# Optimization experiments

Hardware: AMD Instinct MI355X
Metric: run time of the kernel (lower is better)

The kernel has to match this reference:

```python
import jax, jax.numpy as jnp
import numpy as np

N_NODES = 50000
N_EDGES = 800000
IN_C = 512
OUT_C = 256
DEC_D = 256
MASK_RATE = 0.5
NUM_MASK = int(N_NODES * MASK_RATE)


def _gcn_conv(h_in, W, b, src, dst, dinv, n):
    # PyG GCNConv: add self-loops, symmetric normalization D^-1/2 (A+I) D^-1/2
    h = h_in @ W                                   # [N, out]
    coef = (dinv[src] * dinv[dst])[:, None]        # [E, 1]
    agg = jax.ops.segment_sum(h[src] * coef, dst, num_segments=n)
    agg = agg + h * (dinv * dinv)[:, None]         # self-loop term
    return agg + b


def setup_inputs() -> dict:
    key = jax.random.key(0)
    ks = jax.random.split(key, 9)
    x = jax.random.normal(ks[0], (N_NODES, IN_C), dtype=jnp.float32)
    edge_index = jax.random.randint(ks[1], (2, N_EDGES), 0, N_NODES, dtype=jnp.int32)
    perm = jax.random.permutation(ks[2], N_NODES)
    mask_indices = perm[:NUM_MASK].astype(jnp.int32)
    mask_token = jax.random.normal(ks[3], (1, IN_C), dtype=jnp.float32)
    s_enc = 1.0 / np.sqrt(IN_C)
    enc_W = jax.random.uniform(ks[4], (IN_C, OUT_C), jnp.float32, -s_enc, s_enc)
    enc_b = jnp.zeros((OUT_C,), jnp.float32)
    s_dec = 1.0 / np.sqrt(OUT_C)
    dec_W = jax.random.uniform(ks[5], (OUT_C, DEC_D), jnp.float32, -s_dec, s_dec)
    dec_b = jnp.zeros((DEC_D,), jnp.float32)
    s_mlp = 1.0 / np.sqrt(DEC_D)
    mlp_W = jax.random.uniform(ks[6], (DEC_D, IN_C), jnp.float32, -s_mlp, s_mlp)
    mlp_b = jax.random.uniform(ks[7], (IN_C,), jnp.float32, -s_mlp, s_mlp)
    return {"x": x, "edge_index": edge_index, "mask_indices": mask_indices,
            "mask_token": mask_token, "enc_W": enc_W, "enc_b": enc_b,
            "dec_W": dec_W, "dec_b": dec_b, "mlp_W": mlp_W, "mlp_b": mlp_b}


def reference(x, edge_index, mask_indices, mask_token, enc_W, enc_b, dec_W, dec_b, mlp_W, mlp_b):
    src, dst = edge_index[0], edge_index[1]
    n = x.shape[0]
    # degree with self-loops (shared by both GCN layers)
    deg = jax.ops.segment_sum(jnp.ones((N_EDGES,), x.dtype), dst, num_segments=n) + 1.0
    dinv = jax.lax.rsqrt(deg)
    # mask nodes: replace masked rows with learned mask token
    x_masked = x.at[mask_indices].set(mask_token[0])
    # encoder: GCNConv(in_c -> out_c)
    z = _gcn_conv(x_masked, enc_W, enc_b, src, dst, dinv, n)
    # decoder: GCNConv(out_c -> dec_d) -> relu -> linear(dec_d -> in_c)
    h = jax.nn.relu(_gcn_conv(z, dec_W, dec_b, src, dst, dinv, n))
    x_recon = h @ mlp_W + mlp_b
    return (x_recon, x, mask_indices)
```

## Files before the change

kernel.cpp:

```cpp
#include <hip/hip_runtime.h>
#include <math.h>

#define NNODES 50000
#define NEDGES 800000
#define INC 512
#define OUTC 256
#define DECD 256
#define NMASK 25000

#define SCAN_B 1024
#define NSCAN ((NNODES + SCAN_B - 1) / SCAN_B)

#define PB_CVT   25000
#define PB_DEG   (PB_CVT + 3125)
#define PB_MASK  (PB_DEG + 98)
#define PB_WT    (PB_MASK + 1280)
#define PB_TOK   (PB_WT + 64)

typedef __attribute__((ext_vector_type(8))) short short8;
typedef __attribute__((ext_vector_type(4))) float f32x4;

__device__ __forceinline__ unsigned short f2bf(float f) {
    unsigned int u = __float_as_uint(f);
    u = (u + 0x7fff + ((u >> 16) & 1)) >> 16;
    return (unsigned short)u;
}
__device__ __forceinline__ float bf2f(unsigned short u) {
    return __uint_as_float(((unsigned int)u) << 16);
}


__global__ __launch_bounds__(256) void prep_k(const float4* __restrict__ x4,
                                              float4* __restrict__ outx,
                                              ushort4* __restrict__ xbf,
                                              const int* __restrict__ dst, int* __restrict__ deg,
                                              const int* __restrict__ midx,
                                              float* __restrict__ out_mask,
                                              unsigned* __restrict__ maskbits,
                                              const float* __restrict__ encW,
                                              const float* __restrict__ decW,
                                              const float* __restrict__ mlpW,
                                              unsigned short* __restrict__ encWt,
                                              unsigned short* __restrict__ decWt,
                                              unsigned short* __restrict__ mlpWt,
                                              const float* __restrict__ token,
                                              float* __restrict__ tokh) {
    int b = blockIdx.x, tid = threadIdx.x;
    if (b < PB_CVT) {
        int i = b * 256 + tid;
        float4 v = x4[i];
        outx[i] = v;
        ushort4 u;
        u.x = f2bf(v.x); u.y = f2bf(v.y); u.z = f2bf(v.z); u.w = f2bf(v.w);
        xbf[i] = u;
    } else if (b < PB_DEG) {
        int e = (b - PB_CVT) * 256 + tid;
        atomicAdd(&deg[dst[e]], 1);
    } else if (b < PB_MASK) {
        int i = (b - PB_DEG) * 256 + tid;
        if (i < NMASK) {
            int r = midx[i];
            out_mask[i] = (float)r;
            atomicOr(&maskbits[r >> 5], 1u << (r & 31));
        }
    } else if (b < PB_WT) {
        int o = (b - PB_MASK) * 256 + tid;
        if (o < 131072) {
            int n = o >> 9, k = o & 511;
            encWt[o] = f2bf(encW[(size_t)k * OUTC + n]);
        } else if (o < 196608) {
            int o2 = o - 131072;
            int n = o2 >> 8, k = o2 & 255;
            decWt[o2] = f2bf(decW[(size_t)k * DECD + n]);
        } else {
            int o2 = o - 196608;
            int n = o2 >> 8, k = o2 & 255;
            mlpWt[o2] = f2bf(mlpW[(size_t)k * INC + n]);
        }
    } else {
        int b2 = b - PB_WT;
        int j = b2 * 4 + (tid >> 6);
        int l = tid & 63;
        float s = 0.f;
#pragma unroll
        for (int i = 0; i < INC / 64; ++i) {
            int k = i * 64 + l;
            s += token[k] * encW[(size_t)k * OUTC + j];
        }
#pragma unroll
        for (int d = 32; d > 0; d >>= 1) s += __shfl_down(s, d, 64);
        if (l == 0) tokh[j] = s;
    }
}


__global__ __launch_bounds__(1024) void scan_part_k(const int* __restrict__ deg,
                                                    int* __restrict__ bsum,
                                                    float* __restrict__ dinv) {
    int i = blockIdx.x * SCAN_B + threadIdx.x;
    int v = (i < NNODES) ? deg[i] : 0;
    if (i < NNODES) dinv[i] = rsqrtf((float)v + 1.0f);
    int lane = threadIdx.x & 63, w = threadIdx.x >> 6;
    int s = v;
#pragma unroll
    for (int d = 32; d > 0; d >>= 1) s += __shfl_down(s, d, 64);
    __shared__ int ws[16];
    if (lane == 0) ws[w] = s;
    __syncthreads();
    if (threadIdx.x == 0) {
        int tot = 0;
#pragma unroll
        for (int j = 0; j < 16; ++j) tot += ws[j];
        bsum[blockIdx.x] = tot;
    }
}

__global__ __launch_bounds__(64) void scan_carry_k(const int* __restrict__ bsum,
                                                   int* __restrict__ bcarry,
                                                   int* __restrict__ offs) {
    int t = threadIdx.x;
    int v = (t < NSCAN) ? bsum[t] : 0;
    int incl = v;
#pragma unroll
    for (int d = 1; d < 64; d <<= 1) {
        int u = __shfl_up(incl, d, 64);
        if (t >= d) incl += u;
    }
    if (t < NSCAN) bcarry[t] = incl - v;
    if (t == 63) offs[NNODES] = incl;
}

__global__ __launch_bounds__(1024) void scan_fin_k(const int* __restrict__ deg,
                                                   const int* __restrict__ bcarry,
                                                   int* __restrict__ offs,
                                                   int* __restrict__ cursor) {
    int i = blockIdx.x * SCAN_B + threadIdx.x;
    int v = (i < NNODES) ? deg[i] : 0;
    int lane = threadIdx.x & 63, w = threadIdx.x >> 6;
    int incl = v;
#pragma unroll
    for (int d = 1; d < 64; d <<= 1) {
        int u = __shfl_up(incl, d, 64);
        if (lane >= d) incl += u;
    }
    __shared__ int ws[16];
    if (lane == 63) ws[w] = incl;
    __syncthreads();
    int carry = bcarry[blockIdx.x];
    for (int j = 0; j < w; ++j) carry += ws[j];
    int ex = carry + incl - v;
    if (i < NNODES) { offs[i] = ex; cursor[i] = ex; }
}

__global__ void fill_csr_k(const int* __restrict__ src, const int* __restrict__ dst,
                           const float* __restrict__ dinv, int* __restrict__ cursor,
                           int2* __restrict__ edges) {
    int e = blockIdx.x * blockDim.x + threadIdx.x;
    if (e >= NEDGES) return;
    int s = src[e], d = dst[e];
    int pos = atomicAdd(&cursor[d], 1);
    edges[pos] = make_int2(s, __float_as_int(dinv[s] * dinv[d]));
}


__global__ __launch_bounds__(256) void gemm_bf16_k(const unsigned short* __restrict__ A,
                                                   const unsigned short* __restrict__ Bt,
                                                   void* __restrict__ Cout,
                                                   int M, int K, int N,
                                                   const float* __restrict__ bias,
                                                   int out_bf16,
                                                   const unsigned* __restrict__ maskbits,
                                                   const float* __restrict__ tokh) {
    __shared__ unsigned short As[128 * 32];
    __shared__ unsigned short Bs[128 * 32];
    const int t = threadIdx.x;
    const int lane = t & 63, wv = t >> 6;
    const int bm = blockIdx.y * 128;
    const int bn = blockIdx.x * 128;
    const int wm = (wv >> 1) * 64, wn = (wv & 1) * 64;
    const int lr = lane & 15, lq = lane >> 4;

    f32x4 acc[4][4] = {};

    for (int k0 = 0; k0 < K; k0 += 32) {
        __syncthreads();
#pragma unroll
        for (int r = 0; r < 2; ++r) {
            int idx = r * 256 + wv * 64 + lane;
            int row = idx >> 2;
            int c8 = (idx & 3) * 8;
            int ga = bm + row;
            if (ga >= M) ga = M - 1;
            const unsigned short* gA = A + (size_t)ga * K + k0 + c8;
            const unsigned short* gB = Bt + (size_t)(bn + row) * K + k0 + c8;
            __builtin_amdgcn_global_load_lds(
                (const __attribute__((address_space(1))) unsigned int*)gA,
                (__attribute__((address_space(3))) unsigned int*)&As[(r * 256 + wv * 64) * 8],
                16, 0, 0);
            __builtin_amdgcn_global_load_lds(
                (const __attribute__((address_space(1))) unsigned int*)gB,
                (__attribute__((address_space(3))) unsigned int*)&Bs[(r * 256 + wv * 64) * 8],
                16, 0, 0);
        }
        __syncthreads();

        short8 av[4], bv[4];
#pragma unroll
        for (int mt = 0; mt < 4; ++mt)
            av[mt] = *(const short8*)&As[(wm + mt * 16 + lr) * 32 + lq * 8];
#pragma unroll
        for (int nt = 0; nt < 4; ++nt)
            bv[nt] = *(const short8*)&Bs[(wn + nt * 16 + lr) * 32 + lq * 8];
#pragma unroll
        for (int mt = 0; mt < 4; ++mt)
#pragma unroll
            for (int nt = 0; nt < 4; ++nt)
                acc[mt][nt] = __builtin_amdgcn_mfma_f32_16x16x32_bf16(
                    av[mt], bv[nt], acc[mt][nt], 0, 0, 0);
    }

    bool mrow[16];
#pragma unroll
    for (int mt = 0; mt < 4; ++mt)
#pragma unroll
        for (int reg = 0; reg < 4; ++reg) {
            int row = bm + wm + mt * 16 + lq * 4 + reg;
            mrow[mt * 4 + reg] = false;
            if (maskbits && row < M)
                mrow[mt * 4 + reg] = (maskbits[row >> 5] >> (row & 31)) & 1;
        }

    float* Cf = (float*)Cout;
    unsigned short* Cb = (unsigned short*)Cout;
#pragma unroll
    for (int nt = 0; nt < 4; ++nt) {
        int col = bn + wn + nt * 16 + lr;
        float bv_ = bias ? bias[col] : 0.f;
        float tk = tokh ? tokh[col] : 0.f;
#pragma unroll
        for (int mt = 0; mt < 4; ++mt) {
            int row0 = bm + wm + mt * 16 + lq * 4;
#pragma unroll
            for (int reg = 0; reg < 4; ++reg) {
                int row = row0 + reg;
                if (row >= M) continue;
                float v = mrow[mt * 4 + reg] ? tk : (acc[mt][nt][reg] + bv_);
                if (out_bf16) Cb[(size_t)row * N + col] = f2bf(v);
                else          Cf[(size_t)row * N + col] = v;
            }
        }
    }
}


__global__ __launch_bounds__(256) void agg_bf_k(const unsigned short* __restrict__ h,
                                                unsigned short* __restrict__ out,
                                                const float* __restrict__ bias,
                                                const float* __restrict__ dinv,
                                                const int* __restrict__ offs,
                                                const int2* __restrict__ edges,
                                                int do_relu) {
    int node = blockIdx.x * 4 + (threadIdx.x >> 6);
    if (node >= NNODES) return;
    int t = threadIdx.x & 63;
    int half = t >> 5;
    int cb = (t & 31) * 8;
    int beg = offs[node], end = offs[node + 1];
    float a[8] = {}, b[8] = {}, c[8] = {}, d[8] = {};
    int e = beg;
    for (; e + 8 <= end; e += 8) {
        int2 ev0 = edges[e + half];
        int2 ev1 = edges[e + 2 + half];
        int2 ev2 = edges[e + 4 + half];
        int2 ev3 = edges[e + 6 + half];
        short8 v0 = *(const short8*)(h + (size_t)ev0.x * OUTC + cb);
        short8 v1 = *(const short8*)(h + (size_t)ev1.x * OUTC + cb);
        short8 v2 = *(const short8*)(h + (size_t)ev2.x * OUTC + cb);
        short8 v3 = *(const short8*)(h + (size_t)ev3.x * OUTC + cb);
        float c0 = __int_as_float(ev0.y);
        float c1 = __int_as_float(ev1.y);
        float c2 = __int_as_float(ev2.y);
        float c3 = __int_as_float(ev3.y);
#pragma unroll
        for (int j = 0; j < 8; ++j) {
            a[j] += bf2f((unsigned short)v0[j]) * c0;
            b[j] += bf2f((unsigned short)v1[j]) * c1;
            c[j] += bf2f((unsigned short)v2[j]) * c2;
            d[j] += bf2f((unsigned short)v3[j]) * c3;
        }
    }
    if (e + 4 <= end) {
        int2 ev0 = edges[e + half];
        int2 ev1 = edges[e + 2 + half];
        short8 v0 = *(const short8*)(h + (size_t)ev0.x * OUTC + cb);
        short8 v1 = *(const short8*)(h + (size_t)ev1.x * OUTC + cb);
        float c0 = __int_as_float(ev0.y);
        float c1 = __int_as_float(ev1.y);
#pragma unroll
        for (int j = 0; j < 8; ++j) {
            a[j] += bf2f((unsigned short)v0[j]) * c0;
            b[j] += bf2f((unsigned short)v1[j]) * c1;
        }
        e += 4;
    }
    if (e + 2 <= end) {
        int2 ev = edges[e + half];
        short8 v = *(const short8*)(h + (size_t)ev.x * OUTC + cb);
        float cc = __int_as_float(ev.y);
#pragma unroll
        for (int j = 0; j < 8; ++j) a[j] += bf2f((unsigned short)v[j]) * cc;
        e += 2;
    }
    if (e < end) {
        int2 ev = edges[e];
        short8 v = *(const short8*)(h + (size_t)ev.x * OUTC + cb);
        float cc = half ? 0.f : __int_as_float(ev.y);
#pragma unroll
        for (int j = 0; j < 8; ++j) a[j] += bf2f((unsigned short)v[j]) * cc;
    }
#pragma unroll
    for (int j = 0; j < 8; ++j) {
        a[j] += b[j];
        c[j] += d[j];
        a[j] += c[j];
        a[j] += __shfl_xor(a[j], 32, 64);
    }
    if (half == 0) {
        float di = dinv[node];
        float sc = di * di;
        short8 hv = *(const short8*)(h + (size_t)node * OUTC + cb);
        float4 bv0 = *(const float4*)(bias + cb);
        float4 bv1 = *(const float4*)(bias + cb + 4);
        float r[8];
#pragma unroll
        for (int j = 0; j < 8; ++j) r[j] = a[j] + bf2f((unsigned short)hv[j]) * sc;
        r[0] += bv0.x; r[1] += bv0.y; r[2] += bv0.z; r[3] += bv0.w;
        r[4] += bv1.x; r[5] += bv1.y; r[6] += bv1.z; r[7] += bv1.w;
        if (do_relu) {
#pragma unroll
            for (int j = 0; j < 8; ++j) r[j] = fmaxf(r[j], 0.f);
        }
        short8 u;
#pragma unroll
        for (int j = 0; j < 8; ++j) u[j] = (short)f2bf(r[j]);
        *(short8*)(out + (size_t)node * OUTC + cb) = u;
    }
}


extern "C" void kernel_launch(void* const* d_in, const int* in_sizes, int n_in,
                              void* d_out, int out_size, void* d_ws, size_t ws_size,
                              hipStream_t stream) {
    const float* x    = (const float*)d_in[0];
    const int*   eidx = (const int*)d_in[1];
    const int*   midx = (const int*)d_in[2];
    const float* mtok = (const float*)d_in[3];
    const float* encW = (const float*)d_in[4];
    const float* encB = (const float*)d_in[5];
    const float* decW = (const float*)d_in[6];
    const float* decB = (const float*)d_in[7];
    const float* mlpW = (const float*)d_in[8];
    const float* mlpB = (const float*)d_in[9];
    const int* srcs = eidx;
    const int* dsts = eidx + NEDGES;

    char* ws = (char*)d_ws;
    unsigned short* x_bf  = (unsigned short*)(ws + 0);
    unsigned short* hA_bf = (unsigned short*)(ws + 51200000);
    unsigned short* hB_bf = (unsigned short*)(ws + 76800000);
    int*      deg      = (int*)     (ws + 102400000);
    unsigned* maskbits = (unsigned*)(ws + 102600000);
    float*    dinv     = (float*)   (ws + 102606400);
    int*      offs     = (int*)     (ws + 102806400);
    int*      cursor   = (int*)     (ws + 103006464);
    int2*     edges    = (int2*)    (ws + 103206528);
    float*    tokh     = (float*)   (ws + 109606528);
    unsigned short* encWt = (unsigned short*)(ws + 109607552);
    unsigned short* decWt = (unsigned short*)(ws + 109869696);
    unsigned short* mlpWt = (unsigned short*)(ws + 110000768);
    int*      bsum     = (int*)     (ws + 110262912);
    int*      bcarry   = (int*)     (ws + 110263168);

    float* out_recon = (float*)d_out;
    float* out_x     = out_recon + (size_t)NNODES * INC;
    float* out_mask  = out_x + (size_t)NNODES * INC;

    hipMemsetAsync(deg, 0, 206400, stream);

    prep_k<<<PB_TOK, 256, 0, stream>>>((const float4*)x, (float4*)out_x, (ushort4*)x_bf,
                                       dsts, deg, midx, out_mask, maskbits,
                                       encW, decW, mlpW, encWt, decWt, mlpWt,
                                       mtok, tokh);

    scan_part_k<<<NSCAN, SCAN_B, 0, stream>>>(deg, bsum, dinv);
    scan_carry_k<<<1, 64, 0, stream>>>(bsum, bcarry, offs);
    scan_fin_k<<<NSCAN, SCAN_B, 0, stream>>>(deg, bcarry, offs, cursor);
    fill_csr_k<<<(NEDGES + 255) / 256, 256, 0, stream>>>(srcs, dsts, dinv, cursor, edges);

    gemm_bf16_k<<<dim3(OUTC / 128, (NNODES + 127) / 128), 256, 0, stream>>>(
        x_bf, encWt, hA_bf, NNODES, INC, OUTC, nullptr, 1, maskbits, tokh);

    agg_bf_k<<<(NNODES + 3) / 4, 256, 0, stream>>>(hA_bf, hB_bf, encB, dinv, offs, edges, 0);

    gemm_bf16_k<<<dim3(DECD / 128, (NNODES + 127) / 128), 256, 0, stream>>>(
        hB_bf, decWt, hA_bf, NNODES, OUTC, DECD, nullptr, 1, nullptr, nullptr);

    agg_bf_k<<<(NNODES + 3) / 4, 256, 0, stream>>>(hA_bf, hB_bf, decB, dinv, offs, edges, 1);

    gemm_bf16_k<<<dim3(INC / 128, (NNODES + 127) / 128), 256, 0, stream>>>(
        hB_bf, mlpWt, out_recon, NNODES, DECD, INC, mlpB, 0, nullptr, nullptr);
}
```

Baseline: 644.9 us.

## Fuse scan carry into scan_fin and co-schedule CSR fill with encoder GEMM

Removes the single-block scan_carry kernel: each scan_fin block now reduces the preceding block sums itself, and block 0 writes the total edge count. The CSR fill is merged into the first GEMM launch as extra blocks, so the atomic-scatter edge work overlaps with the encoder matmul instead of running as a separate serial launch. The intent is to cut launch overhead and idle gaps between small kernels. In exchange, the fused launch mixes heterogeneous blocks, and the specialized GEMM now has its shape and masking hardcoded.

```diff
diff --git a/kernel.cpp b/kernel.cpp
--- a/kernel.cpp
+++ b/kernel.cpp
@@ -16,6 +16,9 @@
 #define PB_MASK  (PB_DEG + 98)
 #define PB_WT    (PB_MASK + 1280)
 #define PB_TOK   (PB_WT + 64)
+
+#define G1_BLOCKS 782
+#define G1F_TOTAL (G1_BLOCKS + 3125)
 
 typedef __attribute__((ext_vector_type(8))) short short8;
 typedef __attribute__((ext_vector_type(4))) float f32x4;
@@ -115,68 +118,68 @@
     }
 }
 
-__global__ __launch_bounds__(64) void scan_carry_k(const int* __restrict__ bsum,
-                                                   int* __restrict__ bcarry,
-                                                   int* __restrict__ offs) {
-    int t = threadIdx.x;
-    int v = (t < NSCAN) ? bsum[t] : 0;
-    int incl = v;
-#pragma unroll
-    for (int d = 1; d < 64; d <<= 1) {
-        int u = __shfl_up(incl, d, 64);
-        if (t >= d) incl += u;
-    }
-    if (t < NSCAN) bcarry[t] = incl - v;
-    if (t == 63) offs[NNODES] = incl;
-}
-
 __global__ __launch_bounds__(1024) void scan_fin_k(const int* __restrict__ deg,
-                                                   const int* __restrict__ bcarry,
+                                                   const int* __restrict__ bsum,
                                                    int* __restrict__ offs,
                                                    int* __restrict__ cursor) {
-    int i = blockIdx.x * SCAN_B + threadIdx.x;
+    __shared__ int carry_s;
+    __shared__ int ws[16];
+    int tid = threadIdx.x;
+    int wv = tid >> 6, lane = tid & 63;
+    if (wv == 0) {
+        int v = (lane < NSCAN && lane < (int)blockIdx.x) ? bsum[lane] : 0;
+#pragma unroll
+        for (int d = 32; d > 0; d >>= 1) v += __shfl_down(v, d, 64);
+        if (lane == 0) carry_s = v;
+    } else if (wv == 1 && blockIdx.x == 0) {
+        int v = (lane < NSCAN) ? bsum[lane] : 0;
+#pragma unroll
+        for (int d = 32; d > 0; d >>= 1) v += __shfl_down(v, d, 64);
+        if (lane == 0) offs[NNODES] = v;
+    }
+    int i = blockIdx.x * SCAN_B + tid;
     int v = (i < NNODES) ? deg[i] : 0;
-    int lane = threadIdx.x & 63, w = threadIdx.x >> 6;
     int incl = v;
 #pragma unroll
     for (int d = 1; d < 64; d <<= 1) {
         int u = __shfl_up(incl, d, 64);
         if (lane >= d) incl += u;
     }
-    __shared__ int ws[16];
-    if (lane == 63) ws[w] = incl;
+    if (lane == 63) ws[wv] = incl;
     __syncthreads();
-    int carry = bcarry[blockIdx.x];
-    for (int j = 0; j < w; ++j) carry += ws[j];
+    int carry = carry_s;
+    for (int j = 0; j < wv; ++j) carry += ws[j];
     int ex = carry + incl - v;
     if (i < NNODES) { offs[i] = ex; cursor[i] = ex; }
 }
 
-__global__ void fill_csr_k(const int* __restrict__ src, const int* __restrict__ dst,
-                           const float* __restrict__ dinv, int* __restrict__ cursor,
-                           int2* __restrict__ edges) {
-    int e = blockIdx.x * blockDim.x + threadIdx.x;
-    if (e >= NEDGES) return;
-    int s = src[e], d = dst[e];
-    int pos = atomicAdd(&cursor[d], 1);
-    edges[pos] = make_int2(s, __float_as_int(dinv[s] * dinv[d]));
-}
-
-
-__global__ __launch_bounds__(256) void gemm_bf16_k(const unsigned short* __restrict__ A,
-                                                   const unsigned short* __restrict__ Bt,
-                                                   void* __restrict__ Cout,
-                                                   int M, int K, int N,
-                                                   const float* __restrict__ bias,
-                                                   int out_bf16,
-                                                   const unsigned* __restrict__ maskbits,
-                                                   const float* __restrict__ tokh) {
+
+__global__ __launch_bounds__(256) void gemm1_fill_k(const unsigned short* __restrict__ A,
+                                                    const unsigned short* __restrict__ Bt,
+                                                    unsigned short* __restrict__ C,
+                                                    const unsigned* __restrict__ maskbits,
+                                                    const float* __restrict__ tokh,
+                                                    const int* __restrict__ src,
+                                                    const int* __restrict__ dst,
+                                                    const float* __restrict__ dinv,
+                                                    int* __restrict__ cursor,
+                                                    int2* __restrict__ edges) {
     __shared__ unsigned short As[128 * 32];
     __shared__ unsigned short Bs[128 * 32];
+    if (blockIdx.x >= G1_BLOCKS) {
+        int e = (blockIdx.x - G1_BLOCKS) * 256 + threadIdx.x;
+        if (e < NEDGES) {
+            int s = src[e], d = dst[e];
+            int pos = atomicAdd(&cursor[d], 1);
+            edges[pos] = make_int2(s, __float_as_int(dinv[s] * dinv[d]));
+        }
+        return;
+    }
+    const int M = NNODES, K = INC, N = OUTC;
     const int t = threadIdx.x;
     const int lane = t & 63, wv = t >> 6;
-    const int bm = blockIdx.y * 128;
-    const int bn = blockIdx.x * 128;
+    const int bm = (blockIdx.x >> 1) * 128;
+    const int bn = (blockIdx.x & 1) * 128;
     const int wm = (wv >> 1) * 64, wn = (wv & 1) * 64;
     const int lr = lane & 15, lq = lane >> 4;
 
@@ -225,10 +228,81 @@
 #pragma unroll
         for (int reg = 0; reg < 4; ++reg) {
             int row = bm + wm + mt * 16 + lq * 4 + reg;
-            mrow[mt * 4 + reg] = false;
-            if (maskbits && row < M)
-                mrow[mt * 4 + reg] = (maskbits[row >> 5] >> (row & 31)) & 1;
-        }
+            mrow[mt * 4 + reg] = (row < M) && ((maskbits[row >> 5] >> (row & 31)) & 1);
+        }
+
+#pragma unroll
+    for (int nt = 0; nt < 4; ++nt) {
+        int col = bn + wn + nt * 16 + lr;
+        float tk = tokh[col];
+#pragma unroll
+        for (int mt = 0; mt < 4; ++mt) {
+            int row0 = bm + wm + mt * 16 + lq * 4;
+#pragma unroll
+            for (int reg = 0; reg < 4; ++reg) {
+                int row = row0 + reg;
+                if (row >= M) continue;
+                float v = mrow[mt * 4 + reg] ? tk : acc[mt][nt][reg];
+                C[(size_t)row * N + col] = f2bf(v);
+            }
+        }
+    }
+}
+
+
+__global__ __launch_bounds__(256) void gemm_bf16_k(const unsigned short* __restrict__ A,
+                                                   const unsigned short* __restrict__ Bt,
+                                                   void* __restrict__ Cout,
+                                                   int M, int K, int N,
+                                                   const float* __restrict__ bias,
+                                                   int out_bf16) {
+    __shared__ unsigned short As[128 * 32];
+    __shared__ unsigned short Bs[128 * 32];
+    const int t = threadIdx.x;
+    const int lane = t & 63, wv = t >> 6;
+    const int bm = blockIdx.y * 128;
+    const int bn = blockIdx.x * 128;
+    const int wm = (wv >> 1) * 64, wn = (wv & 1) * 64;
+    const int lr = lane & 15, lq = lane >> 4;
+
+    f32x4 acc[4][4] = {};
+
+    for (int k0 = 0; k0 < K; k0 += 32) {
+        __syncthreads();
+#pragma unroll
+        for (int r = 0; r < 2; ++r) {
+            int idx = r * 256 + wv * 64 + lane;
+            int row = idx >> 2;
+            int c8 = (idx & 3) * 8;
+            int ga = bm + row;
+            if (ga >= M) ga = M - 1;
+            const unsigned short* gA = A + (size_t)ga * K + k0 + c8;
+            const unsigned short* gB = Bt + (size_t)(bn + row) * K + k0 + c8;
+            __builtin_amdgcn_global_load_lds(
+                (const __attribute__((address_space(1))) unsigned int*)gA,
+                (__attribute__((address_space(3))) unsigned int*)&As[(r * 256 + wv * 64) * 8],
+                16, 0, 0);
+            __builtin_amdgcn_global_load_lds(
+                (const __attribute__((address_space(1))) unsigned int*)gB,
+                (__attribute__((address_space(3))) unsigned int*)&Bs[(r * 256 + wv * 64) * 8],
+                16, 0, 0);
+        }
+        __syncthreads();
+
+        short8 av[4], bv[4];
+#pragma unroll
+        for (int mt = 0; mt < 4; ++mt)
+            av[mt] = *(const short8*)&As[(wm + mt * 16 + lr) * 32 + lq * 8];
+#pragma unroll
+        for (int nt = 0; nt < 4; ++nt)
+            bv[nt] = *(const short8*)&Bs[(wn + nt * 16 + lr) * 32 + lq * 8];
+#pragma unroll
+        for (int mt = 0; mt < 4; ++mt)
+#pragma unroll
+            for (int nt = 0; nt < 4; ++nt)
+                acc[mt][nt] = __builtin_amdgcn_mfma_f32_16x16x32_bf16(
+                    av[mt], bv[nt], acc[mt][nt], 0, 0, 0);
+    }
 
     float* Cf = (float*)Cout;
     unsigned short* Cb = (unsigned short*)Cout;
@@ -236,7 +310,6 @@
     for (int nt = 0; nt < 4; ++nt) {
         int col = bn + wn + nt * 16 + lr;
         float bv_ = bias ? bias[col] : 0.f;
-        float tk = tokh ? tokh[col] : 0.f;
 #pragma unroll
         for (int mt = 0; mt < 4; ++mt) {
             int row0 = bm + wm + mt * 16 + lq * 4;
@@ -244,7 +317,7 @@
             for (int reg = 0; reg < 4; ++reg) {
                 int row = row0 + reg;
                 if (row >= M) continue;
-                float v = mrow[mt * 4 + reg] ? tk : (acc[mt][nt][reg] + bv_);
+                float v = acc[mt][nt][reg] + bv_;
                 if (out_bf16) Cb[(size_t)row * N + col] = f2bf(v);
                 else          Cf[(size_t)row * N + col] = v;
             }
@@ -379,7 +452,6 @@
     unsigned short* decWt = (unsigned short*)(ws + 109869696);
     unsigned short* mlpWt = (unsigned short*)(ws + 110000768);
     int*      bsum     = (int*)     (ws + 110262912);
-    int*      bcarry   = (int*)     (ws + 110263168);
 
     float* out_recon = (float*)d_out;
     float* out_x     = out_recon + (size_t)NNODES * INC;
@@ -393,20 +465,18 @@
                                        mtok, tokh);
 
     scan_part_k<<<NSCAN, SCAN_B, 0, stream>>>(deg, bsum, dinv);
-    scan_carry_k<<<1, 64, 0, stream>>>(bsum, bcarry, offs);
-    scan_fin_k<<<NSCAN, SCAN_B, 0, stream>>>(deg, bcarry, offs, cursor);
-    fill_csr_k<<<(NEDGES + 255) / 256, 256, 0, stream>>>(srcs, dsts, dinv, cursor, edges);
-
-    gemm_bf16_k<<<dim3(OUTC / 128, (NNODES + 127) / 128), 256, 0, stream>>>(
-        x_bf, encWt, hA_bf, NNODES, INC, OUTC, nullptr, 1, maskbits, tokh);
+    scan_fin_k<<<NSCAN, SCAN_B, 0, stream>>>(deg, bsum, offs, cursor);
+
+    gemm1_fill_k<<<G1F_TOTAL, 256, 0, stream>>>(x_bf, encWt, hA_bf, maskbits, tokh,
+                                                srcs, dsts, dinv, cursor, edges);
 
     agg_bf_k<<<(NNODES + 3) / 4, 256, 0, stream>>>(hA_bf, hB_bf, encB, dinv, offs, edges, 0);
 
     gemm_bf16_k<<<dim3(DECD / 128, (NNODES + 127) / 128), 256, 0, stream>>>(
-        hB_bf, decWt, hA_bf, NNODES, OUTC, DECD, nullptr, 1, nullptr, nullptr);
+        hB_bf, decWt, hA_bf, NNODES, OUTC, DECD, nullptr, 1);
 
     agg_bf_k<<<(NNODES + 3) / 4, 256, 0, stream>>>(hA_bf, hB_bf, decB, dinv, offs, edges, 1);
 
     gemm_bf16_k<<<dim3(INC / 128, (NNODES + 127) / 128), 256, 0, stream>>>(
-        hB_bf, mlpWt, out_recon, NNODES, DECD, INC, mlpB, 0, nullptr, nullptr);
-}
+        hB_bf, mlpWt, out_recon, NNODES, DECD, INC, mlpB, 0);
+}
```

Result: faster. 621.3 us (-3.7%).
